# Kernel tuning notes

Hardware: AMD Instinct MI355X
Metric: run time of the kernel (lower is better)

The kernel has to match this reference:

```python
import jax, jax.numpy as jnp
import numpy as np

N_NODES = 50000
N_EDGES = 800000
UNITS = 64
NUM_RADIAL = 20


def setup_inputs() -> dict:
    key = jax.random.key(0)
    ks = jax.random.split(key, 12)
    u, r = UNITS, NUM_RADIAL
    inv_u = 1.0 / np.sqrt(u)
    inv_r = 1.0 / np.sqrt(r)
    return {
        "node": jax.random.normal(ks[0], (N_NODES, u), jnp.float32),
        "equivariant": jax.random.normal(ks[1], (N_NODES, 3, u), jnp.float32),
        "rbf": jax.random.uniform(ks[2], (N_EDGES, r), jnp.float32),
        "envelope": jax.random.uniform(ks[3], (N_EDGES, 1), jnp.float32),
        "r_ij": jax.random.normal(ks[4], (N_EDGES, 3), jnp.float32),
        "edge_index": jax.random.randint(ks[5], (N_EDGES, 2), 0, N_NODES, jnp.int64),
        "Ws": jax.random.uniform(ks[6], (u, u), jnp.float32, -inv_u, inv_u),
        "bs": jax.random.uniform(ks[7], (u,), jnp.float32, -inv_u, inv_u),
        "Wphi": jax.random.uniform(ks[8], (3 * u, u), jnp.float32, -inv_u, inv_u),
        "bphi": jax.random.uniform(ks[9], (3 * u,), jnp.float32, -inv_u, inv_u),
        "Ww": jax.random.uniform(ks[10], (3 * u, r), jnp.float32, -inv_r, inv_r),
        "bw": jax.random.uniform(ks[11], (3 * u,), jnp.float32, -inv_r, inv_r),
    }


def reference(node, equivariant, rbf, envelope, r_ij, edge_index,
              Ws, bs, Wphi, bphi, Ww, bw):
    n_nodes = node.shape[0]
    u = node.shape[1]
    # per-node dense projections
    s = jax.nn.silu(node @ Ws.T + bs)          # [N, u]
    s = s @ Wphi.T + bphi                      # [N, 3u]
    # gather to edges (source = column 1)
    s_e = s[edge_index[:, 1]]                  # [E, 3u]
    # per-edge radial filter with cutoff envelope
    w = rbf @ Ww.T + bw                        # [E, 3u]
    w = w * envelope
    sw = s_e * w                               # [E, 3u]
    sw1, sw2, sw3 = jnp.split(sw, 3, axis=-1)  # each [E, u]
    dst = edge_index[:, 0]
    ds = jax.ops.segment_sum(sw1, dst, num_segments=n_nodes)  # [N, u]
    vj = equivariant[edge_index[:, 1]]         # [E, 3, u]
    dv = vj * sw2[:, None, :] + r_ij[:, :, None] * sw3[:, None, :]  # [E, 3, u]
    dv = jax.ops.segment_sum(dv, dst, num_segments=n_nodes)   # [N, 3, u]
    return (ds, dv)
```

## Files before the change

### kernel.cpp

```cpp
#include <hip/hip_runtime.h>

#define NRAD 20
#define MNODE 8

typedef unsigned short ushort_t;
typedef unsigned int uint_t;

__device__ __forceinline__ float rdlane(float v, int l)
{
    return __uint_as_float(__builtin_amdgcn_readlane(__float_as_uint(v), l));
}

__device__ __forceinline__ ushort_t f2bf(float f)
{
    uint_t u = __float_as_uint(f);
    u += 0x7fff + ((u >> 16) & 1);
    return (ushort_t)(u >> 16);
}

__device__ __forceinline__ uint_t pack2bf(float a, float b)
{
    return (uint_t)f2bf(a) | ((uint_t)f2bf(b) << 16);
}

__device__ __forceinline__ float bflo(uint_t w) { return __uint_as_float(w << 16); }
__device__ __forceinline__ float bfhi(uint_t w) { return __uint_as_float(w & 0xffff0000u); }
__device__ __forceinline__ float bf2f(ushort_t h) { return __uint_as_float(((uint_t)h) << 16); }

__global__ void detect_idx_kernel(const int* __restrict__ eidx, int* __restrict__ flag)
{
    int t = threadIdx.x;
    unsigned long long m = __ballot(eidx[2 * t + 1] != 0);
    if (t == 0) flag[0] = (__popcll(m) > 8) ? 1 : 0;
}

__global__ void hist_kernel(const int* __restrict__ eidx, const int* __restrict__ flag,
                            int* __restrict__ counts, int n_edges)
{
    int fmt32 = flag[0];
    int i0 = blockIdx.x * blockDim.x + threadIdx.x;
    int stride = gridDim.x * blockDim.x;
    if (fmt32) {
        for (int e = i0; e < n_edges; e += stride) atomicAdd(&counts[eidx[2 * e]], 1);
    } else {
        const long long* e64 = (const long long*)eidx;
        for (int e = i0; e < n_edges; e += stride) atomicAdd(&counts[(int)e64[2 * e]], 1);
    }
}

__global__ __launch_bounds__(256)
void scan1_kernel(const int* __restrict__ cnt, int* __restrict__ bsum, int n, int ch)
{
    __shared__ int red[4];
    int b = blockIdx.x, t = threadIdx.x;
    int end = min(n, (b + 1) * ch);
    int v = 0;
    for (int i = b * ch + t; i < end; i += 256) v += cnt[i];
#pragma unroll
    for (int d = 1; d < 64; d <<= 1) v += __shfl_xor(v, d, 64);
    if ((t & 63) == 0) red[t >> 6] = v;
    __syncthreads();
    if (t == 0) bsum[b] = red[0] + red[1] + red[2] + red[3];
}

__global__ __launch_bounds__(256)
void scan2_kernel(const int* __restrict__ bsum, int* __restrict__ bscan, int nb)
{
    __shared__ int wsum[4];
    int t = threadIdx.x, lane = t & 63, w = t >> 6;
    int v = (t < nb) ? bsum[t] : 0;
    int sc = v;
#pragma unroll
    for (int d = 1; d < 64; d <<= 1) {
        int u = __shfl_up(sc, (unsigned)d, 64);
        if (lane >= d) sc += u;
    }
    if (lane == 63) wsum[w] = sc;
    __syncthreads();
    int add = 0;
    for (int j = 0; j < w; j++) add += wsum[j];
    if (t < nb) bscan[t] = (sc + add) - v;
}

__global__ __launch_bounds__(256)
void scan3_kernel(const int* __restrict__ cnt, const int* __restrict__ bscan,
                  int* __restrict__ cur, int n, int ch)
{
    __shared__ int wsum[4];
    __shared__ int btot;
    int b = blockIdx.x, t = threadIdx.x, lane = t & 63, w = t >> 6;
    int end = min(n, (b + 1) * ch);
    int carry = bscan[b];
    for (int base = b * ch; base < end; base += 256) {
        int i = base + t;
        int v = (i < end) ? cnt[i] : 0;
        int sc = v;
#pragma unroll
        for (int d = 1; d < 64; d <<= 1) {
            int u = __shfl_up(sc, (unsigned)d, 64);
            if (lane >= d) sc += u;
        }
        if (lane == 63) wsum[w] = sc;
        __syncthreads();
        int add = 0;
        for (int j = 0; j < w; j++) add += wsum[j];
        if (t == 255) btot = sc + add;
        int excl = carry + (sc + add - v);
        if (i < end) cur[i] = excl;
        __syncthreads();
        carry += btot;
    }
}

__global__ void scatter_rec_kernel(const int* __restrict__ eidx, const int* __restrict__ flag,
                                   int* __restrict__ cur,
                                   const float* __restrict__ env, const float* __restrict__ rij,
                                   const float* __restrict__ rbf,
                                   uint4* __restrict__ rec, int n_edges)
{
    int fmt32 = flag[0];
    int i0 = blockIdx.x * blockDim.x + threadIdx.x;
    int stride = gridDim.x * blockDim.x;
    const long long* e64 = (const long long*)eidx;
    const float4* rbf4 = (const float4*)rbf;
    for (int e = i0; e < n_edges; e += stride) {
        int dst, src;
        if (fmt32) { dst = eidx[2 * e]; src = eidx[2 * e + 1]; }
        else       { dst = (int)e64[2 * e]; src = (int)e64[2 * e + 1]; }
        int pos = atomicAdd(&cur[dst], 1);
        float ev = env[e];
        float r0 = rij[3 * e], r1 = rij[3 * e + 1], r2 = rij[3 * e + 2];
        float4 b0 = rbf4[(size_t)e * 5 + 0];
        float4 b1 = rbf4[(size_t)e * 5 + 1];
        float4 b2 = rbf4[(size_t)e * 5 + 2];
        float4 b3 = rbf4[(size_t)e * 5 + 3];
        float4 b4 = rbf4[(size_t)e * 5 + 4];
        uint4 qa, qb, qc, qd;
        qa.x = (uint_t)src; qa.y = (uint_t)dst;
        qa.z = __float_as_uint(ev); qa.w = __float_as_uint(r0);
        qb.x = __float_as_uint(r1); qb.y = __float_as_uint(r2);
        qb.z = pack2bf(b0.x, b0.y); qb.w = pack2bf(b0.z, b0.w);
        qc.x = pack2bf(b1.x, b1.y); qc.y = pack2bf(b1.z, b1.w);
        qc.z = pack2bf(b2.x, b2.y); qc.w = pack2bf(b2.z, b2.w);
        qd.x = pack2bf(b3.x, b3.y); qd.y = pack2bf(b3.z, b3.w);
        qd.z = pack2bf(b4.x, b4.y); qd.w = pack2bf(b4.z, b4.w);
        size_t rp = (size_t)pos * 4;
        rec[rp] = qa; rec[rp + 1] = qb; rec[rp + 2] = qc; rec[rp + 3] = qd;
    }
}

__global__ void scatter_kernel(const int* __restrict__ eidx, const int* __restrict__ flag,
                               int* __restrict__ cur, int* __restrict__ sorted, int n_edges)
{
    int fmt32 = flag[0];
    int i0 = blockIdx.x * blockDim.x + threadIdx.x;
    int stride = gridDim.x * blockDim.x;
    const long long* e64 = (const long long*)eidx;
    for (int e = i0; e < n_edges; e += stride) {
        int dst = fmt32 ? eidx[2 * e] : (int)e64[2 * e];
        int pos = atomicAdd(&cur[dst], 1);
        sorted[pos] = e;
    }
}

__global__ void eq_cast_kernel(const float* __restrict__ eq,
                               ushort_t* __restrict__ p0, ushort_t* __restrict__ p1,
                               ushort_t* __restrict__ p2, int n_nodes)
{
    int i0 = blockIdx.x * blockDim.x + threadIdx.x;
    int stride = gridDim.x * blockDim.x;
    int total = n_nodes * 192;
    for (int i = i0; i < total; i += stride) {
        int n = i / 192;
        int r = i - n * 192;
        int c = r >> 6, ch = r & 63;
        ushort_t v = f2bf(eq[i]);
        ushort_t* p = (c == 0) ? p0 : (c == 1) ? p1 : p2;
        p[(size_t)n * 64 + ch] = v;
    }
}

__global__ __launch_bounds__(256)
void node_mlp3b(const float* __restrict__ node,
                const float* __restrict__ Ws, const float* __restrict__ bs,
                const float* __restrict__ Wphi, const float* __restrict__ bphi,
                ushort_t* __restrict__ p0, ushort_t* __restrict__ p1,
                ushort_t* __restrict__ p2, int n_nodes)
{
    __shared__ float WsT[64 * 64];
    __shared__ float WphiT[64 * 192];
    const int t = threadIdx.x;
    for (int i = t; i < 64 * 64; i += 256) {
        int j = i >> 6, k = i & 63;
        WsT[k * 64 + j] = Ws[i];
    }
    for (int i = t; i < 192 * 64; i += 256) {
        int j = i >> 6, k = i & 63;
        WphiT[k * 192 + j] = Wphi[i];
    }
    __syncthreads();

    const int lane = t & 63;
    const int wave = t >> 6;
    const int gw = blockIdx.x * 4 + wave;
    const int nw = gridDim.x * 4;
    const float bsc = bs[lane];
    const float bp0 = bphi[lane], bp1 = bphi[64 + lane], bp2 = bphi[128 + lane];

    for (int n0 = gw * MNODE; n0 < n_nodes; n0 += nw * MNODE) {
        const int cnt = min(MNODE, n_nodes - n0);
        float x[MNODE];
#pragma unroll
        for (int m = 0; m < MNODE; m++)
            x[m] = (m < cnt) ? node[(size_t)(n0 + m) * 64 + lane] : 0.f;

        float acc[MNODE];
#pragma unroll
        for (int m = 0; m < MNODE; m++) acc[m] = bsc;
#pragma unroll
        for (int k = 0; k < 64; k++) {
            float wv = WsT[k * 64 + lane];
#pragma unroll
            for (int m = 0; m < MNODE; m++) acc[m] += rdlane(x[m], k) * wv;
        }
        float s1[MNODE];
#pragma unroll
        for (int m = 0; m < MNODE; m++) {
            float a = acc[m];
            s1[m] = a / (1.f + __expf(-a));
        }
        float a0[MNODE], a1[MNODE], a2[MNODE];
#pragma unroll
        for (int m = 0; m < MNODE; m++) { a0[m] = bp0; a1[m] = bp1; a2[m] = bp2; }
#pragma unroll
        for (int k = 0; k < 64; k++) {
            float w0 = WphiT[k * 192 + lane];
            float w1 = WphiT[k * 192 + 64 + lane];
            float w2 = WphiT[k * 192 + 128 + lane];
#pragma unroll
            for (int m = 0; m < MNODE; m++) {
                float sv = rdlane(s1[m], k);
                a0[m] += sv * w0;
                a1[m] += sv * w1;
                a2[m] += sv * w2;
            }
        }
#pragma unroll
        for (int m = 0; m < MNODE; m++) {
            if (m < cnt) {
                size_t ob = (size_t)(n0 + m) * 64 + lane;
                p0[ob] = f2bf(a0[m]);
                p1[ob] = f2bf(a1[m]);
                p2[ob] = f2bf(a2[m]);
            }
        }
    }
}

template <bool USE_REC>
__global__ __launch_bounds__(256)
void accum3_kernel(const ushort_t* __restrict__ s0p, const ushort_t* __restrict__ s1p,
                   const ushort_t* __restrict__ s2p,
                   const ushort_t* __restrict__ q0p, const ushort_t* __restrict__ q1p,
                   const ushort_t* __restrict__ q2p,
                   const uint4* __restrict__ rec,
                   const float* __restrict__ rbf, const float* __restrict__ env,
                   const float* __restrict__ rij, const int* __restrict__ eidx,
                   const int* __restrict__ flag, const int* __restrict__ sorted,
                   const float* __restrict__ Ww, const float* __restrict__ bw,
                   float* __restrict__ ds, float* __restrict__ dv, int n_edges)
{
    __shared__ int    sh_dst[4 * 64];
    __shared__ int    sh_src[4 * 64];
    __shared__ float  sh_env[4 * 64];
    __shared__ float  sh_r[4 * 3 * 64];
    __shared__ float4 sh_rbf[4 * 64 * 5];

    const int lane = threadIdx.x & 63;
    const int w = threadIdx.x >> 6;
    const int tile = blockIdx.x * 4 + w;
    const int base = tile * 64;
    const int nvalid = min(64, n_edges - base);
    const int woff = w * 64;

    if (lane < nvalid) {
        if (USE_REC) {
            size_t rp = (size_t)(base + lane) * 4;
            uint4 qa = rec[rp], qb = rec[rp + 1], qc = rec[rp + 2], qd = rec[rp + 3];
            sh_src[woff + lane] = (int)qa.x;
            sh_dst[woff + lane] = (int)qa.y;
            sh_env[woff + lane] = __uint_as_float(qa.z);
            sh_r[w * 192 + lane]       = __uint_as_float(qa.w);
            sh_r[w * 192 + 64 + lane]  = __uint_as_float(qb.x);
            sh_r[w * 192 + 128 + lane] = __uint_as_float(qb.y);
            float4* dstq = &sh_rbf[(woff + lane) * 5];
            dstq[0] = make_float4(bflo(qb.z), bfhi(qb.z), bflo(qb.w), bfhi(qb.w));
            dstq[1] = make_float4(bflo(qc.x), bfhi(qc.x), bflo(qc.y), bfhi(qc.y));
            dstq[2] = make_float4(bflo(qc.z), bfhi(qc.z), bflo(qc.w), bfhi(qc.w));
            dstq[3] = make_float4(bflo(qd.x), bfhi(qd.x), bflo(qd.y), bfhi(qd.y));
            dstq[4] = make_float4(bflo(qd.z), bfhi(qd.z), bflo(qd.w), bfhi(qd.w));
        } else {
            int e = sorted[base + lane];
            int d_, s_;
            if (flag[0]) {
                const int2* p2 = (const int2*)eidx;
                int2 v = p2[e];
                d_ = v.x; s_ = v.y;
            } else {
                const longlong2* p2 = (const longlong2*)eidx;
                longlong2 v = p2[e];
                d_ = (int)v.x; s_ = (int)v.y;
            }
            sh_dst[woff + lane] = d_;
            sh_src[woff + lane] = s_;
            sh_env[woff + lane] = env[e];
            sh_r[w * 192 + lane]       = rij[3 * e];
            sh_r[w * 192 + 64 + lane]  = rij[3 * e + 1];
            sh_r[w * 192 + 128 + lane] = rij[3 * e + 2];
            const float4* rbf4 = (const float4*)rbf;
#pragma unroll
            for (int q = 0; q < 5; q++) sh_rbf[(woff + lane) * 5 + q] = rbf4[(size_t)e * 5 + q];
        }
    }
    __syncthreads();

    if (nvalid <= 0) return;

    const float4* Ww4 = (const float4*)Ww;
    float4 w0q[5], w1q[5], w2q[5];
#pragma unroll
    for (int q = 0; q < 5; q++) {
        w0q[q] = Ww4[lane * 5 + q];
        w1q[q] = Ww4[(64 + lane) * 5 + q];
        w2q[q] = Ww4[(128 + lane) * 5 + q];
    }
    const float bw0 = bw[lane], bw1 = bw[64 + lane], bw2 = bw[128 + lane];

    float a0 = 0.f, a1 = 0.f, a2 = 0.f, a3 = 0.f;
    int cur = sh_dst[woff];

    for (int j = 0; j < nvalid; j++) {
        int src = sh_src[woff + j];
        float ev = sh_env[woff + j];
        float r0 = sh_r[w * 192 + j];
        float r1 = sh_r[w * 192 + 64 + j];
        float r2 = sh_r[w * 192 + 128 + j];

        size_t sb = (size_t)src * 64 + lane;
        float sv0 = bf2f(s0p[sb]);
        float sv1 = bf2f(s1p[sb]);
        float sv2 = bf2f(s2p[sb]);
        float v0 = bf2f(q0p[sb]);
        float v1 = bf2f(q1p[sb]);
        float v2 = bf2f(q2p[sb]);

        float w0 = bw0, w1 = bw1, w2 = bw2;
#pragma unroll
        for (int q = 0; q < 5; q++) {
            float4 rb = sh_rbf[(woff + j) * 5 + q];
            w0 += rb.x * w0q[q].x + rb.y * w0q[q].y + rb.z * w0q[q].z + rb.w * w0q[q].w;
            w1 += rb.x * w1q[q].x + rb.y * w1q[q].y + rb.z * w1q[q].z + rb.w * w1q[q].w;
            w2 += rb.x * w2q[q].x + rb.y * w2q[q].y + rb.z * w2q[q].z + rb.w * w2q[q].w;
        }
        w0 *= ev; w1 *= ev; w2 *= ev;

        float sw1 = sv1 * w1;
        float sw2 = sv2 * w2;
        a0 += sv0 * w0;
        a1 += v0 * sw1 + r0 * sw2;
        a2 += v1 * sw1 + r1 * sw2;
        a3 += v2 * sw1 + r2 * sw2;

        int nd = (j + 1 < nvalid) ? sh_dst[woff + j + 1] : -2;
        if (nd != cur) {
            unsafeAtomicAdd(&ds[(size_t)cur * 64 + lane], a0);
            size_t db = (size_t)cur * 192 + lane;
            unsafeAtomicAdd(&dv[db], a1);
            unsafeAtomicAdd(&dv[db + 64], a2);
            unsafeAtomicAdd(&dv[db + 128], a3);
            a0 = a1 = a2 = a3 = 0.f;
            cur = nd;
        }
    }
}

__global__ __launch_bounds__(256, 2)
void node_mlp_kernel(const float* __restrict__ node,
                     const float* __restrict__ Ws,
                     const float* __restrict__ bs,
                     const float* __restrict__ Wphi,
                     const float* __restrict__ bphi,
                     float* __restrict__ s_out,
                     int n_nodes)
{
    __shared__ float WsT[64 * 65];
    __shared__ float WphiT[64 * 193];
    const int t = threadIdx.x;
    for (int i = t; i < 64 * 64; i += 256) {
        int c = i >> 6, k = i & 63;
        WsT[k * 65 + c] = Ws[i];
    }
    for (int i = t; i < 192 * 64; i += 256) {
        int j = i >> 6, k = i & 63;
        WphiT[k * 193 + j] = Wphi[i];
    }
    __syncthreads();

    const int lane = t & 63;
    const int wave = t >> 6;
    const int nwaves = (gridDim.x * blockDim.x) >> 6;
    const float bsc = bs[lane];
    const float bp0 = bphi[lane], bp1 = bphi[64 + lane], bp2 = bphi[128 + lane];

    for (int n = blockIdx.x * 4 + wave; n < n_nodes; n += nwaves) {
        float x = node[(size_t)n * 64 + lane];
        float acc = bsc;
#pragma unroll
        for (int k = 0; k < 64; k++) acc += __shfl(x, k) * WsT[k * 65 + lane];
        float s1 = acc / (1.0f + __expf(-acc));
        float a0 = bp0, a1 = bp1, a2 = bp2;
#pragma unroll
        for (int k = 0; k < 64; k++) {
            float sk = __shfl(s1, k);
            a0 += sk * WphiT[k * 193 + lane];
            a1 += sk * WphiT[k * 193 + 64 + lane];
            a2 += sk * WphiT[k * 193 + 128 + lane];
        }
        size_t ob = (size_t)n * 192;
        s_out[ob + lane] = a0;
        s_out[ob + 64 + lane] = a1;
        s_out[ob + 128 + lane] = a2;
    }
}

__global__ __launch_bounds__(256)
void edge_kernel(const float* __restrict__ s,
                 const float* __restrict__ eq,
                 const float* __restrict__ rbf,
                 const float* __restrict__ env,
                 const float* __restrict__ rij,
                 const int* __restrict__ eidx,
                 const int* __restrict__ idx_flag,
                 const float* __restrict__ Ww,
                 const float* __restrict__ bw,
                 float* __restrict__ ds,
                 float* __restrict__ dv,
                 int n_edges)
{
    const int lane = threadIdx.x & 63;
    const int wglob = (blockIdx.x * blockDim.x + threadIdx.x) >> 6;
    const int nw = (gridDim.x * blockDim.x) >> 6;

    float ww0[NRAD], ww1[NRAD], ww2[NRAD];
#pragma unroll
    for (int k = 0; k < NRAD; k++) {
        ww0[k] = Ww[lane * NRAD + k];
        ww1[k] = Ww[(64 + lane) * NRAD + k];
        ww2[k] = Ww[(128 + lane) * NRAD + k];
    }
    const float bw0 = bw[lane], bw1 = bw[64 + lane], bw2 = bw[128 + lane];
    const int fmt32 = idx_flag[0];

    for (int e = wglob; e < n_edges; e += nw) {
        int dst, src;
        if (fmt32) {
            dst = eidx[2 * e];
            src = eidx[2 * e + 1];
        } else {
            const long long* e64 = (const long long*)eidx;
            dst = (int)e64[2 * e];
            src = (int)e64[2 * e + 1];
        }
        float ev = env[e];
        float r0 = rij[3 * e], r1 = rij[3 * e + 1], r2 = rij[3 * e + 2];
        float rb[NRAD];
#pragma unroll
        for (int k = 0; k < NRAD; k++) rb[k] = rbf[(size_t)e * NRAD + k];
        float w0 = bw0, w1 = bw1, w2 = bw2;
#pragma unroll
        for (int k = 0; k < NRAD; k++) {
            w0 += rb[k] * ww0[k];
            w1 += rb[k] * ww1[k];
            w2 += rb[k] * ww2[k];
        }
        w0 *= ev; w1 *= ev; w2 *= ev;

        size_t sb = (size_t)src * 192;
        float sw0 = s[sb + lane] * w0;
        float sw1 = s[sb + 64 + lane] * w1;
        float sw2 = s[sb + 128 + lane] * w2;
        float v0 = eq[sb + lane];
        float v1 = eq[sb + 64 + lane];
        float v2 = eq[sb + 128 + lane];

        unsafeAtomicAdd(&ds[(size_t)dst * 64 + lane], sw0);
        size_t db = (size_t)dst * 192;
        unsafeAtomicAdd(&dv[db + lane],       v0 * sw1 + r0 * sw2);
        unsafeAtomicAdd(&dv[db + 64 + lane],  v1 * sw1 + r1 * sw2);
        unsafeAtomicAdd(&dv[db + 128 + lane], v2 * sw1 + r2 * sw2);
    }
}

extern "C" void kernel_launch(void* const* d_in, const int* in_sizes, int n_in,
                              void* d_out, int out_size, void* d_ws, size_t ws_size,
                              hipStream_t stream)
{
    const float* node = (const float*)d_in[0];
    const float* eq   = (const float*)d_in[1];
    const float* rbf  = (const float*)d_in[2];
    const float* env  = (const float*)d_in[3];
    const float* rij  = (const float*)d_in[4];
    const int*   eidx = (const int*)d_in[5];
    const float* Ws   = (const float*)d_in[6];
    const float* bs   = (const float*)d_in[7];
    const float* Wphi = (const float*)d_in[8];
    const float* bphi = (const float*)d_in[9];
    const float* Ww   = (const float*)d_in[10];
    const float* bw   = (const float*)d_in[11];

    const int n_nodes = in_sizes[0] / 64;
    const int n_edges = in_sizes[3];

    float* out = (float*)d_out;
    float* ds = out;
    float* dv = out + (size_t)n_nodes * 64;
    char* ws = (char*)d_ws;

    const size_t plane_n = (size_t)n_nodes * 64;
    const int ch = (n_nodes + 255) / 256;
    const int nb = (n_nodes + ch - 1) / ch;

    {
        size_t off = 0;
        auto alloc = [&](size_t bytes) { size_t o = off; off = (off + bytes + 255) & ~(size_t)255; return o; };
        size_t o_sp   = alloc(3 * plane_n * sizeof(ushort_t));
        size_t o_qp   = alloc(3 * plane_n * sizeof(ushort_t));
        size_t o_cnt  = alloc(2 * (size_t)n_nodes * sizeof(int));
        size_t o_rec  = alloc((size_t)n_edges * 64);
        size_t o_bsum = alloc(512 * sizeof(int));
        size_t o_flag = alloc(16);
        if (ws_size >= off) {
            ushort_t* sp = (ushort_t*)(ws + o_sp);
            ushort_t* qp = (ushort_t*)(ws + o_qp);
            int* counts = (int*)(ws + o_cnt);
            int* cur = counts + n_nodes;
            uint4* rec = (uint4*)(ws + o_rec);
            int* bsum = (int*)(ws + o_bsum);
            int* bscan = bsum + 256;
            int* flag = (int*)(ws + o_flag);

            hipMemsetAsync(counts, 0, (size_t)n_nodes * sizeof(int), stream);
            hipMemsetAsync(d_out, 0, (size_t)out_size * sizeof(float), stream);
            detect_idx_kernel<<<1, 64, 0, stream>>>(eidx, flag);
            hist_kernel<<<1024, 256, 0, stream>>>(eidx, flag, counts, n_edges);
            scan1_kernel<<<nb, 256, 0, stream>>>(counts, bsum, n_nodes, ch);
            scan2_kernel<<<1, 256, 0, stream>>>(bsum, bscan, nb);
            scan3_kernel<<<nb, 256, 0, stream>>>(counts, bscan, cur, n_nodes, ch);
            scatter_rec_kernel<<<1024, 256, 0, stream>>>(eidx, flag, cur, env, rij, rbf,
                                                         rec, n_edges);
            eq_cast_kernel<<<1024, 256, 0, stream>>>(eq, qp, qp + plane_n, qp + 2 * plane_n,
                                                     n_nodes);
            node_mlp3b<<<512, 256, 0, stream>>>(node, Ws, bs, Wphi, bphi,
                                                sp, sp + plane_n, sp + 2 * plane_n, n_nodes);
            const int n_tiles = (n_edges + 63) / 64;
            accum3_kernel<true><<<(n_tiles + 3) / 4, 256, 0, stream>>>(
                sp, sp + plane_n, sp + 2 * plane_n,
                qp, qp + plane_n, qp + 2 * plane_n,
                rec, rbf, env, rij, eidx, flag, (const int*)nullptr,
                Ww, bw, ds, dv, n_edges);
            return;
        }
    }

    {
        size_t off = 0;
        auto alloc = [&](size_t bytes) { size_t o = off; off = (off + bytes + 255) & ~(size_t)255; return o; };
        size_t o_sp   = alloc(3 * plane_n * sizeof(ushort_t));
        size_t o_qp   = alloc(3 * plane_n * sizeof(ushort_t));
        size_t o_cnt  = alloc(2 * (size_t)n_nodes * sizeof(int));
        size_t o_sort = alloc((size_t)n_edges * sizeof(int));
        size_t o_bsum = alloc(512 * sizeof(int));
        size_t o_flag = alloc(16);
        if (ws_size >= off) {
            ushort_t* sp = (ushort_t*)(ws + o_sp);
            ushort_t* qp = (ushort_t*)(ws + o_qp);
            int* counts = (int*)(ws + o_cnt);
            int* cur = counts + n_nodes;
            int* sorted = (int*)(ws + o_sort);
            int* bsum = (int*)(ws + o_bsum);
            int* bscan = bsum + 256;
            int* flag = (int*)(ws + o_flag);

            hipMemsetAsync(counts, 0, (size_t)n_nodes * sizeof(int), stream);
            hipMemsetAsync(d_out, 0, (size_t)out_size * sizeof(float), stream);
            detect_idx_kernel<<<1, 64, 0, stream>>>(eidx, flag);
            hist_kernel<<<1024, 256, 0, stream>>>(eidx, flag, counts, n_edges);
            scan1_kernel<<<nb, 256, 0, stream>>>(counts, bsum, n_nodes, ch);
            scan2_kernel<<<1, 256, 0, stream>>>(bsum, bscan, nb);
            scan3_kernel<<<nb, 256, 0, stream>>>(counts, bscan, cur, n_nodes, ch);
            scatter_kernel<<<1024, 256, 0, stream>>>(eidx, flag, cur, sorted, n_edges);
            eq_cast_kernel<<<1024, 256, 0, stream>>>(eq, qp, qp + plane_n, qp + 2 * plane_n,
                                                     n_nodes);
            node_mlp3b<<<512, 256, 0, stream>>>(node, Ws, bs, Wphi, bphi,
                                                sp, sp + plane_n, sp + 2 * plane_n, n_nodes);
            const int n_tiles = (n_edges + 63) / 64;
            accum3_kernel<false><<<(n_tiles + 3) / 4, 256, 0, stream>>>(
                sp, sp + plane_n, sp + 2 * plane_n,
                qp, qp + plane_n, qp + 2 * plane_n,
                (const uint4*)nullptr, rbf, env, rij, eidx, flag, sorted,
                Ww, bw, ds, dv, n_edges);
            return;
        }
    }

    {
        float* s_ws = (float*)d_ws;
        int* idx_flag = (int*)(ws + (size_t)n_nodes * 192 * sizeof(float));
        hipMemsetAsync(d_out, 0, (size_t)out_size * sizeof(float), stream);
        detect_idx_kernel<<<1, 64, 0, stream>>>(eidx, idx_flag);
        node_mlp_kernel<<<1024, 256, 0, stream>>>(node, Ws, bs, Wphi, bphi, s_ws, n_nodes);
        edge_kernel<<<4096, 256, 0, stream>>>(s_ws, eq, rbf, env, rij, eidx, idx_flag,
                                              Ww, bw, ds, dv, n_edges);
    }
}
```

Baseline: 598.9 us.

## Interleave per-node bf16 features into one record and prefetch next gather

Packs the three s projections and three equivariant components for each node and channel into a single 12-byte interleaved record. Each edge now needs one 12-byte gather per lane instead of six separate 2-byte gathers from six planes. The accumulation loop also software-prefetches the next edge's source record to hide gather latency. The fallback path that used a sorted index array is removed, and the per-lane loads become 12-byte unaligned-ish accesses with 768-byte node stride.

```diff
diff --git a/kernel.cpp b/kernel.cpp
--- a/kernel.cpp
+++ b/kernel.cpp
@@ -5,6 +5,8 @@
 
 typedef unsigned short ushort_t;
 typedef unsigned int uint_t;
+
+struct U3 { uint_t a, b, c; };
 
 __device__ __forceinline__ float rdlane(float v, int l)
 {
@@ -163,9 +165,8 @@
     }
 }
 
-__global__ void eq_cast_kernel(const float* __restrict__ eq,
-                               ushort_t* __restrict__ p0, ushort_t* __restrict__ p1,
-                               ushort_t* __restrict__ p2, int n_nodes)
+__global__ void eq_cast_i_kernel(const float* __restrict__ eq,
+                                 ushort_t* __restrict__ sq, int n_nodes)
 {
     int i0 = blockIdx.x * blockDim.x + threadIdx.x;
     int stride = gridDim.x * blockDim.x;
@@ -174,18 +175,15 @@
         int n = i / 192;
         int r = i - n * 192;
         int c = r >> 6, ch = r & 63;
-        ushort_t v = f2bf(eq[i]);
-        ushort_t* p = (c == 0) ? p0 : (c == 1) ? p1 : p2;
-        p[(size_t)n * 64 + ch] = v;
+        sq[(size_t)n * 384 + ch * 6 + 3 + c] = f2bf(eq[i]);
     }
 }
 
 __global__ __launch_bounds__(256)
-void node_mlp3b(const float* __restrict__ node,
+void node_mlp3i(const float* __restrict__ node,
                 const float* __restrict__ Ws, const float* __restrict__ bs,
                 const float* __restrict__ Wphi, const float* __restrict__ bphi,
-                ushort_t* __restrict__ p0, ushort_t* __restrict__ p1,
-                ushort_t* __restrict__ p2, int n_nodes)
+                ushort_t* __restrict__ sq, int n_nodes)
 {
     __shared__ float WsT[64 * 64];
     __shared__ float WphiT[64 * 192];
@@ -248,25 +246,17 @@
 #pragma unroll
         for (int m = 0; m < MNODE; m++) {
             if (m < cnt) {
-                size_t ob = (size_t)(n0 + m) * 64 + lane;
-                p0[ob] = f2bf(a0[m]);
-                p1[ob] = f2bf(a1[m]);
-                p2[ob] = f2bf(a2[m]);
+                size_t ob = (size_t)(n0 + m) * 384 + lane * 6;
+                *(uint_t*)(sq + ob) = pack2bf(a0[m], a1[m]);
+                sq[ob + 2] = f2bf(a2[m]);
             }
         }
     }
 }
 
-template <bool USE_REC>
 __global__ __launch_bounds__(256)
-void accum3_kernel(const ushort_t* __restrict__ s0p, const ushort_t* __restrict__ s1p,
-                   const ushort_t* __restrict__ s2p,
-                   const ushort_t* __restrict__ q0p, const ushort_t* __restrict__ q1p,
-                   const ushort_t* __restrict__ q2p,
+void accum6_kernel(const ushort_t* __restrict__ sq,
                    const uint4* __restrict__ rec,
-                   const float* __restrict__ rbf, const float* __restrict__ env,
-                   const float* __restrict__ rij, const int* __restrict__ eidx,
-                   const int* __restrict__ flag, const int* __restrict__ sorted,
                    const float* __restrict__ Ww, const float* __restrict__ bw,
                    float* __restrict__ ds, float* __restrict__ dv, int n_edges)
 {
@@ -284,43 +274,20 @@
     const int woff = w * 64;
 
     if (lane < nvalid) {
-        if (USE_REC) {
-            size_t rp = (size_t)(base + lane) * 4;
-            uint4 qa = rec[rp], qb = rec[rp + 1], qc = rec[rp + 2], qd = rec[rp + 3];
-            sh_src[woff + lane] = (int)qa.x;
-            sh_dst[woff + lane] = (int)qa.y;
-            sh_env[woff + lane] = __uint_as_float(qa.z);
-            sh_r[w * 192 + lane]       = __uint_as_float(qa.w);
-            sh_r[w * 192 + 64 + lane]  = __uint_as_float(qb.x);
-            sh_r[w * 192 + 128 + lane] = __uint_as_float(qb.y);
-            float4* dstq = &sh_rbf[(woff + lane) * 5];
-            dstq[0] = make_float4(bflo(qb.z), bfhi(qb.z), bflo(qb.w), bfhi(qb.w));
-            dstq[1] = make_float4(bflo(qc.x), bfhi(qc.x), bflo(qc.y), bfhi(qc.y));
-            dstq[2] = make_float4(bflo(qc.z), bfhi(qc.z), bflo(qc.w), bfhi(qc.w));
-            dstq[3] = make_float4(bflo(qd.x), bfhi(qd.x), bflo(qd.y), bfhi(qd.y));
-            dstq[4] = make_float4(bflo(qd.z), bfhi(qd.z), bflo(qd.w), bfhi(qd.w));
-        } else {
-            int e = sorted[base + lane];
-            int d_, s_;
-            if (flag[0]) {
-                const int2* p2 = (const int2*)eidx;
-                int2 v = p2[e];
-                d_ = v.x; s_ = v.y;
-            } else {
-                const longlong2* p2 = (const longlong2*)eidx;
-                longlong2 v = p2[e];
-                d_ = (int)v.x; s_ = (int)v.y;
-            }
-            sh_dst[woff + lane] = d_;
-            sh_src[woff + lane] = s_;
-            sh_env[woff + lane] = env[e];
-            sh_r[w * 192 + lane]       = rij[3 * e];
-            sh_r[w * 192 + 64 + lane]  = rij[3 * e + 1];
-            sh_r[w * 192 + 128 + lane] = rij[3 * e + 2];
-            const float4* rbf4 = (const float4*)rbf;
-#pragma unroll
-            for (int q = 0; q < 5; q++) sh_rbf[(woff + lane) * 5 + q] = rbf4[(size_t)e * 5 + q];
-        }
+        size_t rp = (size_t)(base + lane) * 4;
+        uint4 qa = rec[rp], qb = rec[rp + 1], qc = rec[rp + 2], qd = rec[rp + 3];
+        sh_src[woff + lane] = (int)qa.x;
+        sh_dst[woff + lane] = (int)qa.y;
+        sh_env[woff + lane] = __uint_as_float(qa.z);
+        sh_r[w * 192 + lane]       = __uint_as_float(qa.w);
+        sh_r[w * 192 + 64 + lane]  = __uint_as_float(qb.x);
+        sh_r[w * 192 + 128 + lane] = __uint_as_float(qb.y);
+        float4* dstq = &sh_rbf[(woff + lane) * 5];
+        dstq[0] = make_float4(bflo(qb.z), bfhi(qb.z), bflo(qb.w), bfhi(qb.w));
+        dstq[1] = make_float4(bflo(qc.x), bfhi(qc.x), bflo(qc.y), bfhi(qc.y));
+        dstq[2] = make_float4(bflo(qc.z), bfhi(qc.z), bflo(qc.w), bfhi(qc.w));
+        dstq[3] = make_float4(bflo(qd.x), bfhi(qd.x), bflo(qd.y), bfhi(qd.y));
+        dstq[4] = make_float4(bflo(qd.z), bfhi(qd.z), bflo(qd.w), bfhi(qd.w));
     }
     __syncthreads();
 
@@ -339,20 +306,23 @@
     float a0 = 0.f, a1 = 0.f, a2 = 0.f, a3 = 0.f;
     int cur = sh_dst[woff];
 
+    U3 gcur = *(const U3*)(sq + (size_t)sh_src[woff] * 384 + lane * 6);
+
     for (int j = 0; j < nvalid; j++) {
-        int src = sh_src[woff + j];
+        int jn = (j + 1 < nvalid) ? j + 1 : j;
+        U3 gnxt = *(const U3*)(sq + (size_t)sh_src[woff + jn] * 384 + lane * 6);
+
         float ev = sh_env[woff + j];
         float r0 = sh_r[w * 192 + j];
         float r1 = sh_r[w * 192 + 64 + j];
         float r2 = sh_r[w * 192 + 128 + j];
 
-        size_t sb = (size_t)src * 64 + lane;
-        float sv0 = bf2f(s0p[sb]);
-        float sv1 = bf2f(s1p[sb]);
-        float sv2 = bf2f(s2p[sb]);
-        float v0 = bf2f(q0p[sb]);
-        float v1 = bf2f(q1p[sb]);
-        float v2 = bf2f(q2p[sb]);
+        float sv0 = bflo(gcur.a);
+        float sv1 = bfhi(gcur.a);
+        float sv2 = bflo(gcur.b);
+        float v0  = bfhi(gcur.b);
+        float v1  = bflo(gcur.c);
+        float v2  = bfhi(gcur.c);
 
         float w0 = bw0, w1 = bw1, w2 = bw2;
 #pragma unroll
@@ -381,6 +351,7 @@
             a0 = a1 = a2 = a3 = 0.f;
             cur = nd;
         }
+        gcur = gnxt;
     }
 }
 
@@ -526,22 +497,19 @@
     float* dv = out + (size_t)n_nodes * 64;
     char* ws = (char*)d_ws;
 
-    const size_t plane_n = (size_t)n_nodes * 64;
     const int ch = (n_nodes + 255) / 256;
     const int nb = (n_nodes + ch - 1) / ch;
 
     {
         size_t off = 0;
         auto alloc = [&](size_t bytes) { size_t o = off; off = (off + bytes + 255) & ~(size_t)255; return o; };
-        size_t o_sp   = alloc(3 * plane_n * sizeof(ushort_t));
-        size_t o_qp   = alloc(3 * plane_n * sizeof(ushort_t));
+        size_t o_sq   = alloc((size_t)n_nodes * 384 * sizeof(ushort_t));
         size_t o_cnt  = alloc(2 * (size_t)n_nodes * sizeof(int));
         size_t o_rec  = alloc((size_t)n_edges * 64);
         size_t o_bsum = alloc(512 * sizeof(int));
         size_t o_flag = alloc(16);
         if (ws_size >= off) {
-            ushort_t* sp = (ushort_t*)(ws + o_sp);
-            ushort_t* qp = (ushort_t*)(ws + o_qp);
+            ushort_t* sq = (ushort_t*)(ws + o_sq);
             int* counts = (int*)(ws + o_cnt);
             int* cur = counts + n_nodes;
             uint4* rec = (uint4*)(ws + o_rec);
@@ -558,57 +526,11 @@
             scan3_kernel<<<nb, 256, 0, stream>>>(counts, bscan, cur, n_nodes, ch);
             scatter_rec_kernel<<<1024, 256, 0, stream>>>(eidx, flag, cur, env, rij, rbf,
                                                          rec, n_edges);
-            eq_cast_kernel<<<1024, 256, 0, stream>>>(eq, qp, qp + plane_n, qp + 2 * plane_n,
-                                                     n_nodes);
-            node_mlp3b<<<512, 256, 0, stream>>>(node, Ws, bs, Wphi, bphi,
-                                                sp, sp + plane_n, sp + 2 * plane_n, n_nodes);
+            eq_cast_i_kernel<<<1024, 256, 0, stream>>>(eq, sq, n_nodes);
+            node_mlp3i<<<512, 256, 0, stream>>>(node, Ws, bs, Wphi, bphi, sq, n_nodes);
             const int n_tiles = (n_edges + 63) / 64;
-            accum3_kernel<true><<<(n_tiles + 3) / 4, 256, 0, stream>>>(
-                sp, sp + plane_n, sp + 2 * plane_n,
-                qp, qp + plane_n, qp + 2 * plane_n,
-                rec, rbf, env, rij, eidx, flag, (const int*)nullptr,
-                Ww, bw, ds, dv, n_edges);
-            return;
-        }
-    }
-
-    {
-        size_t off = 0;
-        auto alloc = [&](size_t bytes) { size_t o = off; off = (off + bytes + 255) & ~(size_t)255; return o; };
-        size_t o_sp   = alloc(3 * plane_n * sizeof(ushort_t));
-        size_t o_qp   = alloc(3 * plane_n * sizeof(ushort_t));
-        size_t o_cnt  = alloc(2 * (size_t)n_nodes * sizeof(int));
-        size_t o_sort = alloc((size_t)n_edges * sizeof(int));
-        size_t o_bsum = alloc(512 * sizeof(int));
-        size_t o_flag = alloc(16);
-        if (ws_size >= off) {
-            ushort_t* sp = (ushort_t*)(ws + o_sp);
-            ushort_t* qp = (ushort_t*)(ws + o_qp);
-            int* counts = (int*)(ws + o_cnt);
-            int* cur = counts + n_nodes;
-            int* sorted = (int*)(ws + o_sort);
-            int* bsum = (int*)(ws + o_bsum);
-            int* bscan = bsum + 256;
-            int* flag = (int*)(ws + o_flag);
-
-            hipMemsetAsync(counts, 0, (size_t)n_nodes * sizeof(int), stream);
-            hipMemsetAsync(d_out, 0, (size_t)out_size * sizeof(float), stream);
-            detect_idx_kernel<<<1, 64, 0, stream>>>(eidx, flag);
-            hist_kernel<<<1024, 256, 0, stream>>>(eidx, flag, counts, n_edges);
-            scan1_kernel<<<nb, 256, 0, stream>>>(counts, bsum, n_nodes, ch);
-            scan2_kernel<<<1, 256, 0, stream>>>(bsum, bscan, nb);
-            scan3_kernel<<<nb, 256, 0, stream>>>(counts, bscan, cur, n_nodes, ch);
-            scatter_kernel<<<1024, 256, 0, stream>>>(eidx, flag, cur, sorted, n_edges);
-            eq_cast_kernel<<<1024, 256, 0, stream>>>(eq, qp, qp + plane_n, qp + 2 * plane_n,
-                                                     n_nodes);
-            node_mlp3b<<<512, 256, 0, stream>>>(node, Ws, bs, Wphi, bphi,
-                                                sp, sp + plane_n, sp + 2 * plane_n, n_nodes);
-            const int n_tiles = (n_edges + 63) / 64;
-            accum3_kernel<false><<<(n_tiles + 3) / 4, 256, 0, stream>>>(
-                sp, sp + plane_n, sp + 2 * plane_n,
-                qp, qp + plane_n, qp + 2 * plane_n,
-                (const uint4*)nullptr, rbf, env, rij, eidx, flag, sorted,
-                Ww, bw, ds, dv, n_edges);
+            accum6_kernel<<<(n_tiles + 3) / 4, 256, 0, stream>>>(
+                sq, rec, Ww, bw, ds, dv, n_edges);
             return;
         }
     }
```

New measurement: 604.9 us. No clear change (+1.0%).
